# Kernel tuning notes

Measured on AMD Instinct MI355X. Metric: run time of the kernel, lower is better.

The kernel has to match this reference:

```python
import jax, jax.numpy as jnp
import numpy as np

B, S, C = 2, 4096, 640
HEADS = 10
DH = C // HEADS  # 64
SCALE = 1.0 / np.sqrt(DH).astype(np.float32)


def setup_inputs() -> dict:
    key = jax.random.key(0)
    ks = jax.random.split(key, 5)
    w_std = 0.02
    return {
        "hidden_states": jax.random.normal(ks[0], (B, S, C), dtype=jnp.float32),
        "Wq": jax.random.normal(ks[1], (C, C), dtype=jnp.float32) * w_std,
        "Wk": jax.random.normal(ks[2], (C, C), dtype=jnp.float32) * w_std,
        "Wv": jax.random.normal(ks[3], (C, C), dtype=jnp.float32) * w_std,
        "Wo": jax.random.normal(ks[4], (C, C), dtype=jnp.float32) * w_std,
        "b_out": jnp.zeros((C,), dtype=jnp.float32),
    }


def _split_heads(x):
    # [B, S, C] -> [B, H, S, Dh]
    b, s, c = x.shape
    return x.reshape(b, s, HEADS, DH).transpose(0, 2, 1, 3)


def reference(hidden_states, Wq, Wk, Wv, Wo, b_out):
    residual = hidden_states
    # Linear projections (torch nn.Linear: x @ W.T), to_q/k/v have no bias
    q = jnp.einsum("bsc,dc->bsd", hidden_states, Wq)
    k = jnp.einsum("bsc,dc->bsd", hidden_states, Wk)
    v = jnp.einsum("bsc,dc->bsd", hidden_states, Wv)
    q = _split_heads(q)  # [B, H, S, Dh]
    k = _split_heads(k)
    v = _split_heads(v)
    # get_attention_scores: scaled QK^T + softmax (full O(S^2) matrix)
    scores = jnp.einsum("bhqd,bhkd->bhqk", q, k) * SCALE
    probs = jax.nn.softmax(scores, axis=-1)
    out = jnp.einsum("bhqk,bhkd->bhqd", probs, v)  # [B, H, S, Dh]
    # batch_to_head_dim: [B, H, S, Dh] -> [B, S, C]
    out = out.transpose(0, 2, 1, 3).reshape(hidden_states.shape)
    # to_out[0] Linear (with bias), to_out[1] Dropout = identity at eval
    out = jnp.einsum("bsc,dc->bsd", out, Wo) + b_out
    # residual_connection=True, rescale_output_factor=1.0
    return out + residual
```

## Files before the change

### kernel.cpp

```cpp
#include <hip/hip_runtime.h>
#include <stdint.h>
#include <stddef.h>

#define Bsz 2
#define Ssz 4096
#define Csz 640
#define Hn 10
#define Dh 64

typedef __attribute__((ext_vector_type(8))) short bf16x8;
typedef __attribute__((ext_vector_type(4))) float f32x4;
typedef __attribute__((ext_vector_type(16))) float f32x16;

typedef __attribute__((address_space(1))) void as1_void;
typedef __attribute__((address_space(3))) void as3_void;

__device__ __forceinline__ void async16(const void* g, void* l) {
  __builtin_amdgcn_global_load_lds((as1_void*)(g), (as3_void*)(l), 16, 0, 0);
}

__device__ __forceinline__ ushort f2bf(float f) {
  union { float f; uint32_t u; } v; v.f = f;
  return (ushort)((v.u + 0x7FFFu + ((v.u >> 16) & 1u)) >> 16);
}

__device__ __forceinline__ uint32_t pack_bf16(float lo, float hi) {
  return __builtin_amdgcn_perm(__float_as_uint(hi), __float_as_uint(lo), 0x07060302u);
}

__device__ __forceinline__ float fast_exp2(float x) {
#if __has_builtin(__builtin_amdgcn_exp2f)
  return __builtin_amdgcn_exp2f(x);
#else
  return __exp2f(x);
#endif
}

#define QSCALE 0.1803368801111204f

__global__ __launch_bounds__(256) void cvt_bf16(const float* __restrict__ in,
                                                ushort* __restrict__ out, int n4) {
  int i = blockIdx.x * 256 + threadIdx.x;
  if (i < n4) {
    const float4 v = ((const float4*)in)[i];
    ushort4 o;
    o.x = f2bf(v.x); o.y = f2bf(v.y); o.z = f2bf(v.z); o.w = f2bf(v.w);
    ((ushort4*)out)[i] = o;
  }
}

template<int MODE>
__global__ __launch_bounds__(256) void gemm_k(
    const ushort* __restrict__ A, const ushort* __restrict__ W0,
    const ushort* __restrict__ W1, const ushort* __restrict__ W2,
    ushort* __restrict__ Qh, ushort* __restrict__ Kh, ushort* __restrict__ Vt,
    const float* __restrict__ bias, const float* __restrict__ residual,
    float* __restrict__ outf)
{
  __shared__ ushort As[128 * 64];
  __shared__ ushort Bs[128 * 64];
  const int t = threadIdx.x;
  const int lane = t & 63;
  const int w = t >> 6;
  const int quad = lane >> 4;
  const int l15 = lane & 15;
  const int m0 = blockIdx.x * 128;
  const int wub = t & ~63;

  int n0, mat;
  const ushort* W;
  if (MODE == 0) {
    mat = blockIdx.y / 5;
    n0 = (blockIdx.y % 5) * 128;
    W = (mat == 0) ? W0 : ((mat == 1) ? W1 : W2);
  } else {
    mat = 0;
    n0 = blockIdx.y * 128;
    W = W0;
  }
  const int qm = (w >> 1) * 64;
  const int qn = (w & 1) * 64;

  f32x4 acc[4][4];
  const f32x4 zero4 = {0.f, 0.f, 0.f, 0.f};
#pragma unroll
  for (int i = 0; i < 4; ++i)
#pragma unroll
    for (int j = 0; j < 4; ++j) acc[i][j] = zero4;

  for (int k0 = 0; k0 < Csz; k0 += 64) {
    __syncthreads();
#pragma unroll
    for (int s = 0; s < 4; ++s) {
      int L = s * 256 + t;
      int row = L >> 3, pc = L & 7;
      int c = pc ^ (row & 7);
      async16(A + (size_t)(m0 + row) * Csz + k0 + c * 8,
              (char*)As + (s * 256 + wub) * 16);
    }
#pragma unroll
    for (int s = 0; s < 4; ++s) {
      int L = s * 256 + t;
      int row = L >> 3, pc = L & 7;
      int c = pc ^ (row & 7);
      async16(W + (size_t)(n0 + row) * Csz + k0 + c * 8,
              (char*)Bs + (s * 256 + wub) * 16);
    }
    __syncthreads();
#pragma unroll
    for (int ks = 0; ks < 2; ++ks) {
      bf16x8 af[4], bfr[4];
#pragma unroll
      for (int i = 0; i < 4; ++i) {
        int row = qm + i * 16 + l15;
        int pc = (ks * 4 + quad) ^ (row & 7);
        af[i] = *(const bf16x8*)(As + row * 64 + pc * 8);
      }
#pragma unroll
      for (int j = 0; j < 4; ++j) {
        int row = qn + j * 16 + l15;
        int pc = (ks * 4 + quad) ^ (row & 7);
        bfr[j] = *(const bf16x8*)(Bs + row * 64 + pc * 8);
      }
#pragma unroll
      for (int i = 0; i < 4; ++i)
#pragma unroll
        for (int j = 0; j < 4; ++j)
          acc[i][j] = __builtin_amdgcn_mfma_f32_16x16x32_bf16(af[i], bfr[j], acc[i][j], 0, 0, 0);
    }
  }

  if (MODE == 0) {
    if (mat < 2) {
      ushort* __restrict__ dst = (mat == 0) ? Qh : Kh;
      const float sc = (mat == 0) ? QSCALE : 1.0f;
#pragma unroll
      for (int j = 0; j < 4; ++j) {
        int n = n0 + qn + j * 16 + l15;
        int h = n >> 6, dh = n & 63;
#pragma unroll
        for (int i = 0; i < 4; ++i) {
#pragma unroll
          for (int r = 0; r < 4; ++r) {
            int m = m0 + qm + i * 16 + quad * 4 + r;
            int b = m >> 12, sidx = m & 4095;
            dst[(((size_t)b * Hn + h) * Ssz + sidx) * Dh + dh] = f2bf(acc[i][j][r] * sc);
          }
        }
      }
    } else {
#pragma unroll
      for (int j = 0; j < 4; ++j) {
        int n = n0 + qn + j * 16 + l15;
        int h = n >> 6, dh = n & 63;
#pragma unroll
        for (int i = 0; i < 4; ++i) {
          int mb = m0 + qm + i * 16 + quad * 4;
          int b = mb >> 12, sidx = mb & 4095;
          ushort4 pk;
          pk.x = f2bf(acc[i][j][0]); pk.y = f2bf(acc[i][j][1]);
          pk.z = f2bf(acc[i][j][2]); pk.w = f2bf(acc[i][j][3]);
          *(ushort4*)(Vt + (((size_t)b * Hn + h) * Dh + dh) * Ssz + sidx) = pk;
        }
      }
    }
  } else {
#pragma unroll
    for (int j = 0; j < 4; ++j) {
      int n = n0 + qn + j * 16 + l15;
      float bs = bias[n];
#pragma unroll
      for (int i = 0; i < 4; ++i) {
#pragma unroll
        for (int r = 0; r < 4; ++r) {
          int m = m0 + qm + i * 16 + quad * 4 + r;
          size_t idx = (size_t)m * Csz + n;
          outf[idx] = acc[i][j][r] + bs + residual[idx];
        }
      }
    }
  }
}

__global__ __launch_bounds__(128) void attn_k(
    const ushort* __restrict__ Qh, const ushort* __restrict__ Kh,
    const ushort* __restrict__ Vt, ushort* __restrict__ attnb)
{
  __shared__ ushort Ks[64 * 64];
  __shared__ ushort Vs[64 * 64];

  const int t = threadIdx.x;
  const int lane = t & 63;
  const int w = t >> 6;
  const int l31 = lane & 31;
  const int hi = lane >> 5;
  const int wub = t & ~63;
  const int qt = blockIdx.x;
  const int bh = blockIdx.y;
  const int b = bh / Hn, h = bh % Hn;
  const size_t qk_off = (size_t)bh * Ssz * Dh;
  const size_t v_off = (size_t)bh * Dh * Ssz;

  const int q = qt * 64 + w * 32 + l31;

  bf16x8 qf[4];
#pragma unroll
  for (int ks = 0; ks < 4; ++ks)
    qf[ks] = *(const bf16x8*)(Qh + qk_off + (size_t)q * Dh + ks * 16 + hi * 8);

  f32x16 Oa[2];
#pragma unroll
  for (int mt = 0; mt < 2; ++mt)
#pragma unroll
    for (int i = 0; i < 16; ++i) Oa[mt][i] = 0.f;
  float lp0 = 0.f, lp1 = 0.f;

  for (int kv = 0; kv < Ssz; kv += 64) {
    __syncthreads();
#pragma unroll
    for (int s = 0; s < 4; ++s) {
      int L = s * 128 + t;
      int row = L >> 3, pc = L & 7;
      int c = pc ^ (row & 7);
      async16(Kh + qk_off + (size_t)(kv + row) * Dh + c * 8,
              (char*)Ks + (s * 128 + wub) * 16);
    }
#pragma unroll
    for (int s = 0; s < 4; ++s) {
      int L = s * 128 + t;
      int row = L >> 3, pc = L & 7;
      int c = pc ^ (row & 7);
      async16(Vt + v_off + (size_t)row * Ssz + kv + c * 8,
              (char*)Vs + (s * 128 + wub) * 16);
    }
    __syncthreads();

    f32x16 Sa[2];
#pragma unroll
    for (int tau = 0; tau < 2; ++tau) {
#pragma unroll
      for (int i = 0; i < 16; ++i) Sa[tau][i] = 0.f;
      int row = tau * 32 + l31;
#pragma unroll
      for (int ks = 0; ks < 4; ++ks) {
        int pc = (ks * 2 + hi) ^ (row & 7);
        bf16x8 kf = *(const bf16x8*)(Ks + row * 64 + pc * 8);
        Sa[tau] = __builtin_amdgcn_mfma_f32_32x32x16_bf16(kf, qf[ks], Sa[tau], 0, 0, 0);
      }
    }

    uint32_t pk[2][8];
#pragma unroll
    for (int tau = 0; tau < 2; ++tau) {
#pragma unroll
      for (int a = 0; a < 8; ++a) {
        float p0 = fast_exp2(Sa[tau][2 * a]);
        float p1 = fast_exp2(Sa[tau][2 * a + 1]);
        lp0 += p0; lp1 += p1;
        pk[tau][a] = pack_bf16(p0, p1);
      }
    }

#pragma unroll
    for (int ks2 = 0; ks2 < 4; ++ks2) {
      const int ts = ks2 >> 1;
      const int bA = (2 * ks2) & 3;
      const int bB = (2 * ks2 + 1) & 3;
      uint32_t xA0 = pk[ts][2 * bA], xA1 = pk[ts][2 * bA + 1];
      uint32_t xB0 = pk[ts][2 * bB], xB1 = pk[ts][2 * bB + 1];
      uint32_t own0 = hi ? xB0 : xA0, own1 = hi ? xB1 : xA1;
      uint32_t snd0 = hi ? xA0 : xB0, snd1 = hi ? xA1 : xB1;
      uint32_t rcv0 = (uint32_t)__shfl_xor((int)snd0, 32, 64);
      uint32_t rcv1 = (uint32_t)__shfl_xor((int)snd1, 32, 64);
      union { uint32_t u[4]; bf16x8 v; } pf;
      pf.u[0] = hi ? rcv0 : own0;
      pf.u[1] = hi ? rcv1 : own1;
      pf.u[2] = hi ? own0 : rcv0;
      pf.u[3] = hi ? own1 : rcv1;
#pragma unroll
      for (int mt = 0; mt < 2; ++mt) {
        int row = mt * 32 + l31;
        int pc = (ks2 * 2 + hi) ^ (row & 7);
        bf16x8 vf = *(const bf16x8*)(Vs + row * 64 + pc * 8);
        Oa[mt] = __builtin_amdgcn_mfma_f32_32x32x16_bf16(vf, pf.v, Oa[mt], 0, 0, 0);
      }
    }
  }

  float l_part = lp0 + lp1;
  float l_tot = l_part + __shfl_xor(l_part, 32, 64);
  float inv = 1.0f / l_tot;
  ushort* dst = attnb + ((size_t)b * Ssz + q) * Csz + h * Dh;
#pragma unroll
  for (int mt = 0; mt < 2; ++mt) {
#pragma unroll
    for (int g = 0; g < 4; ++g) {
      int dh0 = mt * 32 + 8 * g + 4 * hi;
      float o0 = Oa[mt][4 * g + 0] * inv;
      float o1 = Oa[mt][4 * g + 1] * inv;
      float o2 = Oa[mt][4 * g + 2] * inv;
      float o3 = Oa[mt][4 * g + 3] * inv;
      uint2 val;
      val.x = pack_bf16(o0, o1);
      val.y = pack_bf16(o2, o3);
      *(uint2*)(dst + dh0) = val;
    }
  }
}

extern "C" void kernel_launch(void* const* d_in, const int* in_sizes, int n_in,
                              void* d_out, int out_size, void* d_ws, size_t ws_size,
                              hipStream_t stream) {
  (void)in_sizes; (void)n_in; (void)out_size; (void)ws_size;
  const float* hs = (const float*)d_in[0];
  const float* Wq = (const float*)d_in[1];
  const float* Wk = (const float*)d_in[2];
  const float* Wv = (const float*)d_in[3];
  const float* Wo = (const float*)d_in[4];
  const float* bo = (const float*)d_in[5];
  float* out = (float*)d_out;

  char* ws = (char*)d_ws;
  ushort* Xbf = (ushort*)(ws);
  ushort* Wqb = (ushort*)(ws + 10485760);
  ushort* Wkb = (ushort*)(ws + 10485760 + 819200);
  ushort* Wvb = (ushort*)(ws + 10485760 + 2 * 819200);
  ushort* Wob = (ushort*)(ws + 10485760 + 3 * 819200);
  ushort* Qh  = (ushort*)(ws + 13762560);
  ushort* Kh  = (ushort*)(ws + 13762560 + 10485760);
  ushort* Vt  = (ushort*)(ws + 13762560 + 2 * 10485760);
  ushort* attnb = (ushort*)(ws + 13762560 + 3 * 10485760);

  hipLaunchKernelGGL(cvt_bf16, dim3(5120), dim3(256), 0, stream, hs, Xbf, 1310720);
  hipLaunchKernelGGL(cvt_bf16, dim3(400), dim3(256), 0, stream, Wq, Wqb, 102400);
  hipLaunchKernelGGL(cvt_bf16, dim3(400), dim3(256), 0, stream, Wk, Wkb, 102400);
  hipLaunchKernelGGL(cvt_bf16, dim3(400), dim3(256), 0, stream, Wv, Wvb, 102400);
  hipLaunchKernelGGL(cvt_bf16, dim3(400), dim3(256), 0, stream, Wo, Wob, 102400);

  hipLaunchKernelGGL((gemm_k<0>), dim3(64, 15), dim3(256), 0, stream,
                     Xbf, Wqb, Wkb, Wvb, Qh, Kh, Vt, (const float*)nullptr,
                     (const float*)nullptr, (float*)nullptr);
  hipLaunchKernelGGL(attn_k, dim3(64, 20), dim3(128), 0, stream, Qh, Kh, Vt, attnb);
  hipLaunchKernelGGL((gemm_k<1>), dim3(64, 5), dim3(256), 0, stream,
                     attnb, Wob, (const ushort*)nullptr, (const ushort*)nullptr,
                     (ushort*)nullptr, (ushort*)nullptr, (ushort*)nullptr,
                     bo, hs, out);
}
```

Measured before the change: 271.7 us.

## Single-wave attention blocks with double-buffered async K/V staging

The attention kernel now uses one 64-lane wave per block that handles all 64 queries (two 32-row halves), so each K/V fragment read from LDS feeds two MFMAs. K/V tiles are double-buffered in LDS, and the next tile is prefetched with async global-to-LDS loads while the current one is computed, synchronised by explicit waitcnt instead of __syncthreads. This aims to hide load latency and cut LDS reads and barriers. In exchange it doubles accumulator registers, raises LDS use to 32KB per block, and relies on hand-coded waitcnt values being correct.

New measurement: 378.5 us. +39.3%, slower.

```diff
diff --git a/kernel.cpp b/kernel.cpp
--- a/kernel.cpp
+++ b/kernel.cpp
@@ -182,82 +182,100 @@
   }
 }
 
-__global__ __launch_bounds__(128) void attn_k(
+__global__ __launch_bounds__(64, 2) void attn_k(
     const ushort* __restrict__ Qh, const ushort* __restrict__ Kh,
     const ushort* __restrict__ Vt, ushort* __restrict__ attnb)
 {
-  __shared__ ushort Ks[64 * 64];
-  __shared__ ushort Vs[64 * 64];
-
-  const int t = threadIdx.x;
-  const int lane = t & 63;
-  const int w = t >> 6;
+  __shared__ ushort Ks[2][64 * 64];
+  __shared__ ushort Vs[2][64 * 64];
+
+  const int lane = threadIdx.x;
   const int l31 = lane & 31;
   const int hi = lane >> 5;
-  const int wub = t & ~63;
   const int qt = blockIdx.x;
   const int bh = blockIdx.y;
   const int b = bh / Hn, h = bh % Hn;
   const size_t qk_off = (size_t)bh * Ssz * Dh;
   const size_t v_off = (size_t)bh * Dh * Ssz;
-
-  const int q = qt * 64 + w * 32 + l31;
-
-  bf16x8 qf[4];
-#pragma unroll
-  for (int ks = 0; ks < 4; ++ks)
-    qf[ks] = *(const bf16x8*)(Qh + qk_off + (size_t)q * Dh + ks * 16 + hi * 8);
-
-  f32x16 Oa[2];
-#pragma unroll
-  for (int mt = 0; mt < 2; ++mt)
-#pragma unroll
-    for (int i = 0; i < 16; ++i) Oa[mt][i] = 0.f;
-  float lp0 = 0.f, lp1 = 0.f;
-
-  for (int kv = 0; kv < Ssz; kv += 64) {
-    __syncthreads();
-#pragma unroll
-    for (int s = 0; s < 4; ++s) {
-      int L = s * 128 + t;
-      int row = L >> 3, pc = L & 7;
-      int c = pc ^ (row & 7);
-      async16(Kh + qk_off + (size_t)(kv + row) * Dh + c * 8,
-              (char*)Ks + (s * 128 + wub) * 16);
-    }
-#pragma unroll
-    for (int s = 0; s < 4; ++s) {
-      int L = s * 128 + t;
-      int row = L >> 3, pc = L & 7;
-      int c = pc ^ (row & 7);
-      async16(Vt + v_off + (size_t)row * Ssz + kv + c * 8,
-              (char*)Vs + (s * 128 + wub) * 16);
-    }
-    __syncthreads();
-
-    f32x16 Sa[2];
+  const int qbase = qt * 64;
+
+  bf16x8 qf[2][4];
+#pragma unroll
+  for (int qh = 0; qh < 2; ++qh) {
+    int q = qbase + qh * 32 + l31;
+#pragma unroll
+    for (int ks = 0; ks < 4; ++ks)
+      qf[qh][ks] = *(const bf16x8*)(Qh + qk_off + (size_t)q * Dh + ks * 16 + hi * 8);
+  }
+
+  f32x16 z16;
+#pragma unroll
+  for (int i = 0; i < 16; ++i) z16[i] = 0.f;
+
+  f32x16 Oa[2][2];
+#pragma unroll
+  for (int qh = 0; qh < 2; ++qh)
+#pragma unroll
+    for (int mt = 0; mt < 2; ++mt) Oa[qh][mt] = z16;
+  float lp[2] = {0.f, 0.f};
+
+  const int row8 = lane >> 3;
+  const int pcs = lane & 7;
+#define STAGE(bi, kv)                                                          \
+  {                                                                            \
+    _Pragma("unroll") for (int s = 0; s < 8; ++s) {                            \
+      int row = s * 8 + row8;                                                  \
+      int c = pcs ^ (row & 7);                                                 \
+      async16(Kh + qk_off + (size_t)((kv) + row) * Dh + c * 8,                 \
+              (char*)&Ks[bi][0] + s * 1024);                                   \
+    }                                                                          \
+    _Pragma("unroll") for (int s = 0; s < 8; ++s) {                            \
+      int row = s * 8 + row8;                                                  \
+      int c = pcs ^ (row & 7);                                                 \
+      async16(Vt + v_off + (size_t)row * Ssz + (kv) + c * 8,                   \
+              (char*)&Vs[bi][0] + s * 1024);                                   \
+    }                                                                          \
+  }
+
+  STAGE(0, 0);
+
+  const int NIT = Ssz / 64;
+  for (int it = 0; it < NIT; ++it) {
+    const int cb = it & 1;
+    __builtin_amdgcn_s_waitcnt(0xC07F);
+    if (it + 1 < NIT) {
+      STAGE(it & 1 ? 0 : 1, (it + 1) * 64);
+      __builtin_amdgcn_s_waitcnt(0x4F70);
+    } else {
+      __builtin_amdgcn_s_waitcnt(0x0F70);
+    }
+
+    const ushort* __restrict__ Kc = &Ks[cb][0];
+    const ushort* __restrict__ Vc = &Vs[cb][0];
+
+    uint32_t pk[2][2][8];
 #pragma unroll
     for (int tau = 0; tau < 2; ++tau) {
-#pragma unroll
-      for (int i = 0; i < 16; ++i) Sa[tau][i] = 0.f;
+      f32x16 Sq[2];
       int row = tau * 32 + l31;
 #pragma unroll
       for (int ks = 0; ks < 4; ++ks) {
         int pc = (ks * 2 + hi) ^ (row & 7);
-        bf16x8 kf = *(const bf16x8*)(Ks + row * 64 + pc * 8);
-        Sa[tau] = __builtin_amdgcn_mfma_f32_32x32x16_bf16(kf, qf[ks], Sa[tau], 0, 0, 0);
-      }
-    }
-
-    uint32_t pk[2][8];
-#pragma unroll
-    for (int tau = 0; tau < 2; ++tau) {
-#pragma unroll
-      for (int a = 0; a < 8; ++a) {
-        float p0 = fast_exp2(Sa[tau][2 * a]);
-        float p1 = fast_exp2(Sa[tau][2 * a + 1]);
-        lp0 += p0; lp1 += p1;
-        pk[tau][a] = pack_bf16(p0, p1);
+        bf16x8 kf = *(const bf16x8*)(Kc + row * 64 + pc * 8);
+        Sq[0] = __builtin_amdgcn_mfma_f32_32x32x16_bf16(kf, qf[0][ks],
+                                                        ks == 0 ? z16 : Sq[0], 0, 0, 0);
+        Sq[1] = __builtin_amdgcn_mfma_f32_32x32x16_bf16(kf, qf[1][ks],
+                                                        ks == 0 ? z16 : Sq[1], 0, 0, 0);
+      }
+#pragma unroll
+      for (int qh = 0; qh < 2; ++qh) {
+#pragma unroll
+        for (int a = 0; a < 8; ++a) {
+          float p0 = fast_exp2(Sq[qh][2 * a]);
+          float p1 = fast_exp2(Sq[qh][2 * a + 1]);
+          lp[qh] += p0 + p1;
+          pk[qh][tau][a] = pack_bf16(p0, p1);
+        }
       }
     }
 
@@ -266,44 +284,55 @@
       const int ts = ks2 >> 1;
       const int bA = (2 * ks2) & 3;
       const int bB = (2 * ks2 + 1) & 3;
-      uint32_t xA0 = pk[ts][2 * bA], xA1 = pk[ts][2 * bA + 1];
-      uint32_t xB0 = pk[ts][2 * bB], xB1 = pk[ts][2 * bB + 1];
-      uint32_t own0 = hi ? xB0 : xA0, own1 = hi ? xB1 : xA1;
-      uint32_t snd0 = hi ? xA0 : xB0, snd1 = hi ? xA1 : xB1;
-      uint32_t rcv0 = (uint32_t)__shfl_xor((int)snd0, 32, 64);
-      uint32_t rcv1 = (uint32_t)__shfl_xor((int)snd1, 32, 64);
-      union { uint32_t u[4]; bf16x8 v; } pf;
-      pf.u[0] = hi ? rcv0 : own0;
-      pf.u[1] = hi ? rcv1 : own1;
-      pf.u[2] = hi ? own0 : rcv0;
-      pf.u[3] = hi ? own1 : rcv1;
+      bf16x8 pf[2];
+#pragma unroll
+      for (int qh = 0; qh < 2; ++qh) {
+        uint32_t xA0 = pk[qh][ts][2 * bA], xA1 = pk[qh][ts][2 * bA + 1];
+        uint32_t xB0 = pk[qh][ts][2 * bB], xB1 = pk[qh][ts][2 * bB + 1];
+        uint32_t own0 = hi ? xB0 : xA0, own1 = hi ? xB1 : xA1;
+        uint32_t snd0 = hi ? xA0 : xB0, snd1 = hi ? xA1 : xB1;
+        uint32_t rcv0 = (uint32_t)__shfl_xor((int)snd0, 32, 64);
+        uint32_t rcv1 = (uint32_t)__shfl_xor((int)snd1, 32, 64);
+        union { uint32_t u[4]; bf16x8 v; } pu;
+        pu.u[0] = hi ? rcv0 : own0;
+        pu.u[1] = hi ? rcv1 : own1;
+        pu.u[2] = hi ? own0 : rcv0;
+        pu.u[3] = hi ? own1 : rcv1;
+        pf[qh] = pu.v;
+      }
 #pragma unroll
       for (int mt = 0; mt < 2; ++mt) {
         int row = mt * 32 + l31;
         int pc = (ks2 * 2 + hi) ^ (row & 7);
-        bf16x8 vf = *(const bf16x8*)(Vs + row * 64 + pc * 8);
-        Oa[mt] = __builtin_amdgcn_mfma_f32_32x32x16_bf16(vf, pf.v, Oa[mt], 0, 0, 0);
-      }
-    }
-  }
-
-  float l_part = lp0 + lp1;
-  float l_tot = l_part + __shfl_xor(l_part, 32, 64);
-  float inv = 1.0f / l_tot;
-  ushort* dst = attnb + ((size_t)b * Ssz + q) * Csz + h * Dh;
-#pragma unroll
-  for (int mt = 0; mt < 2; ++mt) {
-#pragma unroll
-    for (int g = 0; g < 4; ++g) {
-      int dh0 = mt * 32 + 8 * g + 4 * hi;
-      float o0 = Oa[mt][4 * g + 0] * inv;
-      float o1 = Oa[mt][4 * g + 1] * inv;
-      float o2 = Oa[mt][4 * g + 2] * inv;
-      float o3 = Oa[mt][4 * g + 3] * inv;
-      uint2 val;
-      val.x = pack_bf16(o0, o1);
-      val.y = pack_bf16(o2, o3);
-      *(uint2*)(dst + dh0) = val;
+        bf16x8 vf = *(const bf16x8*)(Vc + row * 64 + pc * 8);
+        Oa[0][mt] = __builtin_amdgcn_mfma_f32_32x32x16_bf16(vf, pf[0], Oa[0][mt], 0, 0, 0);
+        Oa[1][mt] = __builtin_amdgcn_mfma_f32_32x32x16_bf16(vf, pf[1], Oa[1][mt], 0, 0, 0);
+      }
+    }
+  }
+#undef STAGE
+
+#pragma unroll
+  for (int qh = 0; qh < 2; ++qh) {
+    float l_part = lp[qh];
+    float l_tot = l_part + __shfl_xor(l_part, 32, 64);
+    float inv = 1.0f / l_tot;
+    int q = qbase + qh * 32 + l31;
+    ushort* dst = attnb + ((size_t)b * Ssz + q) * Csz + h * Dh;
+#pragma unroll
+    for (int mt = 0; mt < 2; ++mt) {
+#pragma unroll
+      for (int g = 0; g < 4; ++g) {
+        int dh0 = mt * 32 + 8 * g + 4 * hi;
+        float o0 = Oa[qh][mt][4 * g + 0] * inv;
+        float o1 = Oa[qh][mt][4 * g + 1] * inv;
+        float o2 = Oa[qh][mt][4 * g + 2] * inv;
+        float o3 = Oa[qh][mt][4 * g + 3] * inv;
+        uint2 val;
+        val.x = pack_bf16(o0, o1);
+        val.y = pack_bf16(o2, o3);
+        *(uint2*)(dst + dh0) = val;
+      }
     }
   }
 }
@@ -340,7 +369,7 @@
   hipLaunchKernelGGL((gemm_k<0>), dim3(64, 15), dim3(256), 0, stream,
                      Xbf, Wqb, Wkb, Wvb, Qh, Kh, Vt, (const float*)nullptr,
                      (const float*)nullptr, (float*)nullptr);
-  hipLaunchKernelGGL(attn_k, dim3(64, 20), dim3(128), 0, stream, Qh, Kh, Vt, attnb);
+  hipLaunchKernelGGL(attn_k, dim3(64, 20), dim3(64), 0, stream, Qh, Kh, Vt, attnb);
   hipLaunchKernelGGL((gemm_k<1>), dim3(64, 5), dim3(256), 0, stream,
                      attnb, Wob, (const ushort*)nullptr, (const ushort*)nullptr,
                      (ushort*)nullptr, (ushort*)nullptr, (ushort*)nullptr,
```
